# Optimization experiments

Hardware: AMD Instinct MI355X
Metric: run time of the kernel (lower is better)

Reference implementation:

```python
import jax, jax.numpy as jnp
import numpy as np

N_NODES = 50000
N_EDGES = 800000
IN_FEATS = 128
OUT_FEATS = 128
FREQ_DIM = OUT_FEATS // 2 + 1
BN_EPS = 1e-5


def setup_inputs() -> dict:
    key = jax.random.key(0)
    ks = jax.random.split(key, 8)
    x = jax.random.normal(ks[0], (N_NODES, IN_FEATS), dtype=jnp.float32)
    edge_index = jax.random.randint(ks[1], (2, N_EDGES), 0, N_NODES, dtype=jnp.int64)
    # lin_fusion: Linear(2*in_feats, out_feats)
    W_fuse = jax.random.normal(ks[2], (OUT_FEATS, 2 * IN_FEATS), dtype=jnp.float32) * (1.0 / np.sqrt(2 * IN_FEATS))
    b_fuse = jnp.zeros((OUT_FEATS,), dtype=jnp.float32)
    # lin_in: Linear(in_feats, out_feats)
    W_in = jax.random.normal(ks[3], (OUT_FEATS, IN_FEATS), dtype=jnp.float32) * (1.0 / np.sqrt(IN_FEATS))
    b_in = jnp.zeros((OUT_FEATS,), dtype=jnp.float32)
    complex_weight = jax.random.normal(ks[4], (FREQ_DIM, 2), dtype=jnp.float32) * 0.02
    alpha = jnp.float32(0.5)
    gamma = jnp.ones((OUT_FEATS,), dtype=jnp.float32)
    beta = jnp.zeros((OUT_FEATS,), dtype=jnp.float32)
    return {"x": x, "edge_index": edge_index, "W_fuse": W_fuse, "b_fuse": b_fuse,
            "W_in": W_in, "b_in": b_in, "complex_weight": complex_weight,
            "alpha": alpha, "gamma": gamma, "beta": beta}


def reference(x, edge_index, W_fuse, b_fuse, W_in, b_in, complex_weight, alpha, gamma, beta):
    N = x.shape[0]
    src, dst = edge_index[0], edge_index[1]
    # --- spatial branch: scatter-mean aggregation of neighbor features ---
    msgs = x[src]  # [E, in] gather
    agg_sum = jax.ops.segment_sum(msgs, dst, num_segments=N)  # [N, in]
    cnt = jax.ops.segment_sum(jnp.ones((src.shape[0],), dtype=x.dtype), dst, num_segments=N)
    aggs = agg_sum / jnp.maximum(cnt, 1.0)[:, None]
    combined = jnp.concatenate([x, aggs], axis=1)  # [N, 2*in]
    x_spatial = combined @ W_fuse.T + b_fuse  # [N, out]
    # --- spectral branch: linear -> rfft * complex weight -> irfft ---
    h = x @ W_in.T + b_in  # [N, out]
    hf = jnp.fft.rfft(h, axis=-1)  # [N, out//2+1]
    w = complex_weight[:, 0] + 1j * complex_weight[:, 1]
    x_spectral = jnp.fft.irfft(hf * w, n=h.shape[-1], axis=-1).astype(x.dtype)
    # --- fuse + BatchNorm1d (training stats, biased var) + exact GELU ---
    out = x_spatial + alpha * x_spectral
    mean = jnp.mean(out, axis=0)
    var = jnp.mean(jnp.square(out - mean), axis=0)
    out = (out - mean) / jnp.sqrt(var + BN_EPS) * gamma + beta
    return jax.nn.gelu(out, approximate=False)
```

## Files before the change

### kernel.cpp

```cpp
#include <hip/hip_runtime.h>
#include <hip/hip_bf16.h>

#define NN 50000
#define NE 800000
#define FD 128
#define FREQ 65
#define CAP 64
#define BN_EPS 1e-5f

#define NB_PACK 3125
#define NB_CVT  6250
#define NB_WCB  128
#define NGRP 8
#define GRPN 6250
#define NCHUNK 256
#define CHUNKE 3125

typedef unsigned int u32;
typedef unsigned short u16;
typedef __attribute__((ext_vector_type(8))) short short8;
typedef __attribute__((ext_vector_type(4))) float float4v;
typedef __attribute__((ext_vector_type(2))) float floatx2;

__device__ __forceinline__ float bf2f(u16 v) {
    return __uint_as_float(((u32)v) << 16);
}
__device__ __forceinline__ u16 f2bf(float f) {
    u32 u = __float_as_uint(f);
    u32 lsb = (u >> 16) & 1u;
    return (u16)((u + 0x7fffu + lsb) >> 16);
}
__device__ __forceinline__ float ldf(const void* p, int i, int f32) {
    return f32 ? ((const float*)p)[i] : bf2f(((const u16*)p)[i]);
}
__device__ __forceinline__ int detect_f32(const void* gamma) {
    return ((const u32*)gamma)[0] == 0x3F800000u;
}
__device__ __forceinline__ int detect_idx64(const int* idx) {
    return (idx[1] | idx[3] | idx[5] | idx[7] |
            idx[9] | idx[11] | idx[13] | idx[15]) == 0;
}

__device__ __forceinline__ u32 pk4_e4m3(float a, float b, float c, float d) {
#if __has_builtin(__builtin_amdgcn_cvt_pk_fp8_f32)
    int r = __builtin_amdgcn_cvt_pk_fp8_f32(a, b, 0, false);
    r = __builtin_amdgcn_cvt_pk_fp8_f32(c, d, r, true);
    return (u32)r;
#else
    auto one = [](float f) -> u32 {
        u32 u = __float_as_uint(f);
        u32 s = (u >> 24) & 0x80u;
        float af = fabsf(f);
        if (af > 448.f) return s | 0x7Eu;
        if (af < 7.8125e-3f) return s;
        int e = (int)((u >> 23) & 255) - 127;
        u32 m = (u >> 20) & 7u;
        u32 rnd = (u >> 19) & 1u;
        u32 sticky = (u & 0x7FFFFu) ? 1u : 0u;
        m += (rnd & (sticky | (m & 1u)));
        u32 ee = (u32)(e + 7);
        if (m > 7u) { m = 0u; ee += 1u; }
        if (ee > 15u) return s | 0x7Eu;
        return s | (ee << 3) | m;
    };
    return one(a) | (one(b) << 8) | (one(c) << 16) | (one(d) << 24);
#endif
}
__device__ __forceinline__ void deq4_e4m3(u32 p, float& a, float& b, float& c, float& d) {
#if __has_builtin(__builtin_amdgcn_cvt_pk_f32_fp8)
    floatx2 lo = __builtin_amdgcn_cvt_pk_f32_fp8((int)p, false);
    floatx2 hi = __builtin_amdgcn_cvt_pk_f32_fp8((int)p, true);
    a = lo.x; b = lo.y; c = hi.x; d = hi.y;
#else
    auto one = [](u32 v) -> float {
        u32 s = (v & 0x80u) << 24;
        u32 e = (v >> 3) & 15u;
        u32 m = v & 7u;
        if (e == 0) {
            float f = (float)m * 0.001953125f;
            return s ? -f : f;
        }
        return __uint_as_float(s | ((e + 120u) << 23) | (m << 20));
    };
    a = one(p & 255u); b = one((p >> 8) & 255u);
    c = one((p >> 16) & 255u); d = one(p >> 24);
#endif
}

#define WS_WCB       0
#define WS_BIAS      65536
#define WS_ZSTART    66048
#define WS_BNSUM     66048
#define WS_BNSQ      66560
#define WS_DEG       67072
#define WS_ZEND      267072
#define WS_CSR16     267136
#define WS_AGG16     6667136
#define WS_EPACK     6667136
#define WS_OUT16     19467136
#define WS_X8        19467136

__global__ __launch_bounds__(256) void prep_kernel(const void* __restrict__ x,
                                                   const int* __restrict__ idx,
                                                   const void* __restrict__ Wf,
                                                   const void* __restrict__ bfu,
                                                   const void* __restrict__ Wi,
                                                   const void* __restrict__ bi,
                                                   const void* __restrict__ cw,
                                                   const void* __restrict__ alpha_p,
                                                   const void* __restrict__ gamma,
                                                   u32* __restrict__ epack,
                                                   u32* __restrict__ x8,
                                                   u16* __restrict__ WcB,
                                                   float* __restrict__ bias) {
    int b = blockIdx.x;
    int t = threadIdx.x;
    if (b < NB_PACK) {
        int e = b * 256 + t;
        int src, dst;
        if (detect_idx64(idx)) { src = idx[2 * e]; dst = idx[2 * NE + 2 * e]; }
        else                   { src = idx[e];     dst = idx[NE + e]; }
        epack[e] = ((u32)dst << 16) | (u32)src;
        return;
    }
    b -= NB_PACK;
    if (b < NB_CVT) {
        int gid = b * 256 + t;
        float a, bb, c, d;
        if (detect_f32(gamma)) {
            float4 v = ((const float4*)x)[gid];
            a = v.x; bb = v.y; c = v.z; d = v.w;
        } else {
            uint2 v = ((const uint2*)x)[gid];
            a = bf2f((u16)(v.x & 0xffffu)); bb = bf2f((u16)(v.x >> 16));
            c = bf2f((u16)(v.y & 0xffffu)); d = bf2f((u16)(v.y >> 16));
        }
        x8[gid] = pk4_e4m3(a, bb, c, d);
        return;
    }
    b -= NB_CVT;
    int f32 = detect_f32(gamma);
    int j = b;
    __shared__ float wr[FREQ], wi[FREQ];
    __shared__ float cl[128];
    __shared__ float part[256];
    if (t < FREQ) { wr[t] = ldf(cw, 2 * t, f32); wi[t] = ldf(cw, 2 * t + 1, f32); }
    __syncthreads();
    if (t < 128) {
        float s = wr[0] + ((t & 1) ? -wr[64] : wr[64]);
        for (int f = 1; f < 64; ++f) {
            int ph = (f * t) & 127;
            float th = (float)ph * (6.283185307179586f / 128.f);
            float sn, cs;
            sincosf(th, &sn, &cs);
            s += 2.f * (wr[f] * cs - wi[f] * sn);
        }
        cl[t] = s * (1.f / 128.f);
    }
    __syncthreads();
    int k = t & 127, mh = t >> 7;
    float acc = 0.f;
    int m0 = mh * 64;
#pragma unroll 8
    for (int mm = 0; mm < 64; ++mm) {
        int m = m0 + mm;
        acc = fmaf(ldf(Wi, m * 128 + k, f32), cl[(j - m) & 127], acc);
    }
    part[t] = acc;
    __syncthreads();
    if (t < 128) {
        float al = ldf(alpha_p, 0, f32);
        int ct = j >> 4;
        float v = ldf(Wf, j * 256 + k, f32) + al * (part[k] + part[k + 128]);
        int off = (((ct * 8 + (k >> 5)) * 64) + ((k >> 3) & 3) * 16 + (j & 15)) * 8 + (k & 7);
        WcB[off] = f2bf(v);
        int k2 = k + 128;
        float v2 = ldf(Wf, j * 256 + k2, f32);
        int off2 = (((ct * 8 + (k2 >> 5)) * 64) + ((k2 >> 3) & 3) * 16 + (j & 15)) * 8 + (k2 & 7);
        WcB[off2] = f2bf(v2);
        if (j == 0) {
            float bacc = 0.f;
            for (int m = 0; m < 128; ++m)
                bacc = fmaf(ldf(bi, m, f32), cl[(t - m) & 127], bacc);
            bias[t] = ldf(bfu, t, f32) + al * bacc;
        }
    }
}

__global__ __launch_bounds__(256) void bucket8_kernel(const u32* __restrict__ epack,
                                                      int* __restrict__ deg,
                                                      u16* __restrict__ csr) {
    int g = blockIdx.x & (NGRP - 1);
    int chunk = blockIdx.x >> 3;
    u32 lo = (u32)(g * GRPN) << 16;
    u32 hi = (u32)((g + 1) * GRPN) << 16;
    int base = chunk * CHUNKE;
    for (int i = threadIdx.x; i < CHUNKE; i += 256) {
        u32 p = epack[base + i];
        if (p >= lo && p < hi) {
            int dst = (int)(p >> 16);
            int pos = atomicAdd(deg + dst, 1);
            if (pos < CAP) csr[dst * CAP + pos] = (u16)(p & 0xffffu);
        }
    }
}

__global__ __launch_bounds__(256) void aggregate_kernel(const u32* __restrict__ x8,
                                                        const u16* __restrict__ csr,
                                                        const int* __restrict__ deg,
                                                        u32* __restrict__ agg16) {
    int gid = blockIdx.x * 256 + threadIdx.x;
    int n = gid >> 6;
    int lane = gid & 63;
    if (n >= NN) return;
    int q = lane & 31;
    int half = lane >> 5;
    int s = n * CAP;
    int dcount = deg[n];
    int e = s + min(dcount, CAP);
    float a0 = 0.f, a1 = 0.f, a2 = 0.f, a3 = 0.f;
    int i = s + half;
    for (; i + 2 < e; i += 4) {
        int s0 = csr[i], s1 = csr[i + 2];
        u32 p0 = x8[(size_t)s0 * 32 + q];
        u32 p1 = x8[(size_t)s1 * 32 + q];
        float b0, b1, b2, b3, c0, c1, c2, c3;
        deq4_e4m3(p0, b0, b1, b2, b3);
        deq4_e4m3(p1, c0, c1, c2, c3);
        a0 += b0 + c0; a1 += b1 + c1; a2 += b2 + c2; a3 += b3 + c3;
    }
    if (i < e) {
        u32 p = x8[(size_t)csr[i] * 32 + q];
        float b0, b1, b2, b3;
        deq4_e4m3(p, b0, b1, b2, b3);
        a0 += b0; a1 += b1; a2 += b2; a3 += b3;
    }
    a0 += __shfl_xor(a0, 32); a1 += __shfl_xor(a1, 32);
    a2 += __shfl_xor(a2, 32); a3 += __shfl_xor(a3, 32);
    if (half == 0) {
        float rinv = 1.f / fmaxf((float)dcount, 1.f);
        uint2 w;
        w.x = (u32)f2bf(a0 * rinv) | ((u32)f2bf(a1 * rinv) << 16);
        w.y = (u32)f2bf(a2 * rinv) | ((u32)f2bf(a3 * rinv) << 16);
        ((uint2*)agg16)[(size_t)n * 32 + q] = w;
    }
}

__global__ __launch_bounds__(256) void gemm_kernel(const void* __restrict__ x,
                                                   const u16* __restrict__ agg16,
                                                   const void* __restrict__ gamma,
                                                   const u16* __restrict__ WcB,
                                                   const float* __restrict__ bias,
                                                   u16* __restrict__ outp16,
                                                   float* __restrict__ bnsum,
                                                   float* __restrict__ bnsq) {
    __shared__ float lsum[FD], lsq[FD];
    int t = threadIdx.x;
    if (t < FD) { lsum[t] = 0.f; lsq[t] = 0.f; }
    __syncthreads();
    int f32 = detect_f32(gamma);
    int wave = t >> 6;
    int lane = t & 63;
    int quad = lane >> 4;
    int lm = lane & 15;
    int n0 = blockIdx.x * 64;
    int nrow = n0 + wave * 16 + lm;
    bool avalid = (nrow < NN);

    float4v acc[8];
#pragma unroll
    for (int ct = 0; ct < 8; ++ct) acc[ct] = (float4v){0.f, 0.f, 0.f, 0.f};

    const short8* bp = (const short8*)WcB;
#pragma unroll
    for (int ks = 0; ks < 8; ++ks) {
        short8 a = (short8)0;
        if (avalid) {
            if (ks < 4) {
                int k = ks * 32 + quad * 8;
                if (f32) {
                    const float4* p = (const float4*)x + (size_t)nrow * 32 + (k >> 2);
                    float4 v0 = p[0], v1 = p[1];
                    a[0] = (short)f2bf(v0.x); a[1] = (short)f2bf(v0.y);
                    a[2] = (short)f2bf(v0.z); a[3] = (short)f2bf(v0.w);
                    a[4] = (short)f2bf(v1.x); a[5] = (short)f2bf(v1.y);
                    a[6] = (short)f2bf(v1.z); a[7] = (short)f2bf(v1.w);
                } else {
                    a = ((const short8*)x)[(size_t)nrow * 16 + (k >> 3)];
                }
            } else {
                int k = (ks - 4) * 32 + quad * 8;
                a = ((const short8*)agg16)[(size_t)nrow * 16 + (k >> 3)];
            }
        }
#pragma unroll
        for (int ct = 0; ct < 8; ++ct) {
            short8 b = bp[(ct * 8 + ks) * 64 + lane];
            acc[ct] = __builtin_amdgcn_mfma_f32_16x16x32_bf16(a, b, acc[ct], 0, 0, 0);
        }
    }

    int rbase = n0 + wave * 16 + quad * 4;
#pragma unroll
    for (int ct = 0; ct < 8; ++ct) {
        int col = ct * 16 + lm;
        float bj = bias[col];
        float s = 0.f, q = 0.f;
#pragma unroll
        for (int r = 0; r < 4; ++r) {
            int n = rbase + r;
            if (n < NN) {
                float v = acc[ct][r] + bj;
                outp16[(size_t)n * FD + col] = f2bf(v);
                s += v;
                q = fmaf(v, v, q);
            }
        }
        s += __shfl_xor(s, 16); s += __shfl_xor(s, 32);
        q += __shfl_xor(q, 16); q += __shfl_xor(q, 32);
        if (lane < 16) {
            atomicAdd(&lsum[col], s);
            atomicAdd(&lsq[col], q);
        }
    }
    __syncthreads();
    if (t < FD) {
        atomicAdd(bnsum + t, lsum[t]);
        atomicAdd(bnsq + t, lsq[t]);
    }
}

__global__ __launch_bounds__(256) void apply_kernel(const u32* __restrict__ outp16,
                                                    const float* __restrict__ bnsum,
                                                    const float* __restrict__ bnsq,
                                                    const void* __restrict__ gamma,
                                                    const void* __restrict__ beta,
                                                    void* __restrict__ out) {
    __shared__ float sc[FD], sh[FD];
    int t = threadIdx.x;
    int f32 = detect_f32(gamma);
    if (t < FD) {
        float mean = bnsum[t] * (1.f / NN);
        float var = bnsq[t] * (1.f / NN) - mean * mean;
        float s = ldf(gamma, t, f32) / sqrtf(var + BN_EPS);
        sc[t] = s;
        sh[t] = ldf(beta, t, f32) - mean * s;
    }
    __syncthreads();
    int gid = blockIdx.x * 256 + t;
    if (gid >= NN * (FD / 8)) return;
    uint4 pk = ((const uint4*)outp16)[gid];
    int f0 = (gid * 8) & 127;
    u32 w[4] = {pk.x, pk.y, pk.z, pk.w};
    float g[8];
#pragma unroll
    for (int q = 0; q < 4; ++q) {
        float v0 = bf2f((u16)(w[q] & 0xffffu));
        float v1 = bf2f((u16)(w[q] >> 16));
        float z0 = fmaf(v0, sc[f0 + 2 * q], sh[f0 + 2 * q]);
        float z1 = fmaf(v1, sc[f0 + 2 * q + 1], sh[f0 + 2 * q + 1]);
        g[2 * q]     = 0.5f * z0 * (1.f + erff(z0 * 0.70710678118654752f));
        g[2 * q + 1] = 0.5f * z1 * (1.f + erff(z1 * 0.70710678118654752f));
    }
    if (f32) {
        float4* o = (float4*)out + (size_t)gid * 2;
        o[0] = make_float4(g[0], g[1], g[2], g[3]);
        o[1] = make_float4(g[4], g[5], g[6], g[7]);
    } else {
        uint4 o;
        o.x = (u32)f2bf(g[0]) | ((u32)f2bf(g[1]) << 16);
        o.y = (u32)f2bf(g[2]) | ((u32)f2bf(g[3]) << 16);
        o.z = (u32)f2bf(g[4]) | ((u32)f2bf(g[5]) << 16);
        o.w = (u32)f2bf(g[6]) | ((u32)f2bf(g[7]) << 16);
        ((uint4*)out)[gid] = o;
    }
}

extern "C" void kernel_launch(void* const* d_in, const int* in_sizes, int n_in,
                              void* d_out, int out_size, void* d_ws, size_t ws_size,
                              hipStream_t stream) {
    const void* x     = d_in[0];
    const int* eidx   = (const int*)d_in[1];
    const void* Wf    = d_in[2];
    const void* bfu   = d_in[3];
    const void* Wi    = d_in[4];
    const void* bi    = d_in[5];
    const void* cw    = d_in[6];
    const void* alpha = d_in[7];
    const void* gamma = d_in[8];
    const void* beta  = d_in[9];

    char* ws = (char*)d_ws;
    u16*   WcB    = (u16*)(ws + WS_WCB);
    float* bias   = (float*)(ws + WS_BIAS);
    float* bnsum  = (float*)(ws + WS_BNSUM);
    float* bnsq   = (float*)(ws + WS_BNSQ);
    int*   deg    = (int*)(ws + WS_DEG);
    u16*   csr    = (u16*)(ws + WS_CSR16);
    u32*   epack  = (u32*)(ws + WS_EPACK);
    u32*   agg16  = (u32*)(ws + WS_AGG16);
    u16*   outp16 = (u16*)(ws + WS_OUT16);
    u32*   x8     = (u32*)(ws + WS_X8);

    hipMemsetAsync(ws + WS_ZSTART, 0, (size_t)WS_ZEND - WS_ZSTART, stream);

    prep_kernel<<<NB_PACK + NB_CVT + NB_WCB, 256, 0, stream>>>(
        x, eidx, Wf, bfu, Wi, bi, cw, alpha, gamma, epack, x8, WcB, bias);
    bucket8_kernel<<<NGRP * NCHUNK, 256, 0, stream>>>(epack, deg, csr);
    aggregate_kernel<<<(NN * 64 + 255) / 256, 256, 0, stream>>>(x8, csr, deg, agg16);
    gemm_kernel<<<(NN + 63) / 64, 256, 0, stream>>>(x, (const u16*)agg16, gamma, WcB,
                                                    bias, outp16, bnsum, bnsq);
    apply_kernel<<<(NN * (FD / 8) + 255) / 256, 256, 0, stream>>>((const u32*)outp16,
                                                                  bnsum, bnsq, gamma,
                                                                  beta, d_out);
}
```

Measured before the change: 236.3 us.

## Fuse neighbor aggregation into GEMM kernel via shared-memory staging

Removes the separate aggregate kernel and computes the mean-aggregated neighbor features inside the GEMM block, staging the bf16 results in LDS instead of writing and re-reading them from global memory. CSR indices are loaded once per wave row and broadcast with shuffles, and eight gathers are issued before any dequantization to raise memory-level parallelism. This saves one launch and the agg16 round trip. The cost is lower parallelism for the gather phase (782 blocks, each wave handling 8 nodes serially per half) plus 16KB of LDS per block, which may reduce occupancy.

```diff
diff --git a/kernel.cpp b/kernel.cpp
--- a/kernel.cpp
+++ b/kernel.cpp
@@ -95,10 +95,9 @@
 #define WS_DEG       67072
 #define WS_ZEND      267072
 #define WS_CSR16     267136
-#define WS_AGG16     6667136
 #define WS_EPACK     6667136
-#define WS_OUT16     19467136
-#define WS_X8        19467136
+#define WS_X8        9867136
+#define WS_OUT16     16267136
 
 __global__ __launch_bounds__(256) void prep_kernel(const void* __restrict__ x,
                                                    const int* __restrict__ idx,
@@ -205,49 +204,10 @@
     }
 }
 
-__global__ __launch_bounds__(256) void aggregate_kernel(const u32* __restrict__ x8,
-                                                        const u16* __restrict__ csr,
-                                                        const int* __restrict__ deg,
-                                                        u32* __restrict__ agg16) {
-    int gid = blockIdx.x * 256 + threadIdx.x;
-    int n = gid >> 6;
-    int lane = gid & 63;
-    if (n >= NN) return;
-    int q = lane & 31;
-    int half = lane >> 5;
-    int s = n * CAP;
-    int dcount = deg[n];
-    int e = s + min(dcount, CAP);
-    float a0 = 0.f, a1 = 0.f, a2 = 0.f, a3 = 0.f;
-    int i = s + half;
-    for (; i + 2 < e; i += 4) {
-        int s0 = csr[i], s1 = csr[i + 2];
-        u32 p0 = x8[(size_t)s0 * 32 + q];
-        u32 p1 = x8[(size_t)s1 * 32 + q];
-        float b0, b1, b2, b3, c0, c1, c2, c3;
-        deq4_e4m3(p0, b0, b1, b2, b3);
-        deq4_e4m3(p1, c0, c1, c2, c3);
-        a0 += b0 + c0; a1 += b1 + c1; a2 += b2 + c2; a3 += b3 + c3;
-    }
-    if (i < e) {
-        u32 p = x8[(size_t)csr[i] * 32 + q];
-        float b0, b1, b2, b3;
-        deq4_e4m3(p, b0, b1, b2, b3);
-        a0 += b0; a1 += b1; a2 += b2; a3 += b3;
-    }
-    a0 += __shfl_xor(a0, 32); a1 += __shfl_xor(a1, 32);
-    a2 += __shfl_xor(a2, 32); a3 += __shfl_xor(a3, 32);
-    if (half == 0) {
-        float rinv = 1.f / fmaxf((float)dcount, 1.f);
-        uint2 w;
-        w.x = (u32)f2bf(a0 * rinv) | ((u32)f2bf(a1 * rinv) << 16);
-        w.y = (u32)f2bf(a2 * rinv) | ((u32)f2bf(a3 * rinv) << 16);
-        ((uint2*)agg16)[(size_t)n * 32 + q] = w;
-    }
-}
-
 __global__ __launch_bounds__(256) void gemm_kernel(const void* __restrict__ x,
-                                                   const u16* __restrict__ agg16,
+                                                   const u32* __restrict__ x8,
+                                                   const u16* __restrict__ csr,
+                                                   const int* __restrict__ deg,
                                                    const void* __restrict__ gamma,
                                                    const u16* __restrict__ WcB,
                                                    const float* __restrict__ bias,
@@ -255,15 +215,61 @@
                                                    float* __restrict__ bnsum,
                                                    float* __restrict__ bnsq) {
     __shared__ float lsum[FD], lsq[FD];
+    __shared__ __align__(16) u16 lag[64 * FD];
     int t = threadIdx.x;
     if (t < FD) { lsum[t] = 0.f; lsq[t] = 0.f; }
-    __syncthreads();
     int f32 = detect_f32(gamma);
     int wave = t >> 6;
     int lane = t & 63;
+    int n0 = blockIdx.x * 64;
+
+    {
+        int half = lane >> 5;
+        int q = lane & 31;
+        for (int nn = 0; nn < 8; ++nn) {
+            int lrow = wave * 16 + half * 8 + nn;
+            int node = n0 + lrow;
+            int dcount = 0;
+            u32 cv = 0;
+            if (node < NN) {
+                dcount = deg[node];
+                cv = ((const u32*)csr)[(size_t)node * (CAP / 2) + q];
+            }
+            int cnt = min(dcount, CAP);
+            float a0 = 0.f, a1 = 0.f, a2 = 0.f, a3 = 0.f;
+            int jj = 0;
+            while (jj < cnt) {
+                int nb = cnt - jj;
+                u32 p[8];
+#pragma unroll
+                for (int r = 0; r < 8; ++r) {
+                    if (r < nb) {
+                        u32 w = __shfl(cv, half * 32 + ((jj + r) >> 1));
+                        u16 srcn = (u16)(w >> (((jj + r) & 1) * 16));
+                        p[r] = x8[(size_t)srcn * 32 + q];
+                    }
+                }
+#pragma unroll
+                for (int r = 0; r < 8; ++r) {
+                    if (r < nb) {
+                        float b0, b1, b2, b3;
+                        deq4_e4m3(p[r], b0, b1, b2, b3);
+                        a0 += b0; a1 += b1; a2 += b2; a3 += b3;
+                    }
+                }
+                jj += 8;
+            }
+            float rinv = 1.f / fmaxf((float)dcount, 1.f);
+            uint2 w;
+            w.x = (u32)f2bf(a0 * rinv) | ((u32)f2bf(a1 * rinv) << 16);
+            w.y = (u32)f2bf(a2 * rinv) | ((u32)f2bf(a3 * rinv) << 16);
+            ((uint2*)lag)[lrow * 32 + q] = w;
+        }
+    }
+    __syncthreads();
+
     int quad = lane >> 4;
     int lm = lane & 15;
-    int n0 = blockIdx.x * 64;
     int nrow = n0 + wave * 16 + lm;
     bool avalid = (nrow < NN);
 
@@ -275,8 +281,8 @@
 #pragma unroll
     for (int ks = 0; ks < 8; ++ks) {
         short8 a = (short8)0;
-        if (avalid) {
-            if (ks < 4) {
+        if (ks < 4) {
+            if (avalid) {
                 int k = ks * 32 + quad * 8;
                 if (f32) {
                     const float4* p = (const float4*)x + (size_t)nrow * 32 + (k >> 2);
@@ -288,10 +294,10 @@
                 } else {
                     a = ((const short8*)x)[(size_t)nrow * 16 + (k >> 3)];
                 }
-            } else {
-                int k = (ks - 4) * 32 + quad * 8;
-                a = ((const short8*)agg16)[(size_t)nrow * 16 + (k >> 3)];
             }
+        } else {
+            int k = (ks - 4) * 32 + quad * 8;
+            a = *(const short8*)&lag[(wave * 16 + lm) * FD + k];
         }
 #pragma unroll
         for (int ct = 0; ct < 8; ++ct) {
@@ -398,17 +404,15 @@
     int*   deg    = (int*)(ws + WS_DEG);
     u16*   csr    = (u16*)(ws + WS_CSR16);
     u32*   epack  = (u32*)(ws + WS_EPACK);
-    u32*   agg16  = (u32*)(ws + WS_AGG16);
+    u32*   x8     = (u32*)(ws + WS_X8);
     u16*   outp16 = (u16*)(ws + WS_OUT16);
-    u32*   x8     = (u32*)(ws + WS_X8);
 
     hipMemsetAsync(ws + WS_ZSTART, 0, (size_t)WS_ZEND - WS_ZSTART, stream);
 
     prep_kernel<<<NB_PACK + NB_CVT + NB_WCB, 256, 0, stream>>>(
         x, eidx, Wf, bfu, Wi, bi, cw, alpha, gamma, epack, x8, WcB, bias);
     bucket8_kernel<<<NGRP * NCHUNK, 256, 0, stream>>>(epack, deg, csr);
-    aggregate_kernel<<<(NN * 64 + 255) / 256, 256, 0, stream>>>(x8, csr, deg, agg16);
-    gemm_kernel<<<(NN + 63) / 64, 256, 0, stream>>>(x, (const u16*)agg16, gamma, WcB,
+    gemm_kernel<<<(NN + 63) / 64, 256, 0, stream>>>(x, x8, csr, deg, gamma, WcB,
                                                     bias, outp16, bnsum, bnsq);
     apply_kernel<<<(NN * (FD / 8) + 255) / 256, 256, 0, stream>>>((const u32*)outp16,
                                                                   bnsum, bnsq, gamma,
```

New measurement: 251.8 us. 6.6% more time.

## Preload CSR row via wave shuffle and batch 8 gathers with zero sentinel row

Applied to the files above, without the earlier changes.

The aggregate kernel now loads each node's whole 64-entry CSR row with one coalesced 32-bit load per lane and hands neighbor indices out with shuffles. Eight x8 gathers are issued before any dequantization, and padding slots point at an all-zero sentinel row that an extra memset clears, so the loop needs no tail handling. The workspace is rearranged so x8, agg16 and outp16 no longer alias, which the sentinel row requires. The aim is more memory-level parallelism in the gather. In exchange, nodes whose degree is not a multiple of 16 fetch extra sentinel rows.

```diff
diff --git a/kernel.cpp b/kernel.cpp
--- a/kernel.cpp
+++ b/kernel.cpp
@@ -15,6 +15,7 @@
 #define GRPN 6250
 #define NCHUNK 256
 #define CHUNKE 3125
+#define SENT NN
 
 typedef unsigned int u32;
 typedef unsigned short u16;
@@ -95,10 +96,10 @@
 #define WS_DEG       67072
 #define WS_ZEND      267072
 #define WS_CSR16     267136
-#define WS_AGG16     6667136
 #define WS_EPACK     6667136
-#define WS_OUT16     19467136
-#define WS_X8        19467136
+#define WS_X8        9867136
+#define WS_AGG16     16267264
+#define WS_OUT16     29067264
 
 __global__ __launch_bounds__(256) void prep_kernel(const void* __restrict__ x,
                                                    const int* __restrict__ idx,
@@ -211,34 +212,39 @@
                                                         u32* __restrict__ agg16) {
     int gid = blockIdx.x * 256 + threadIdx.x;
     int n = gid >> 6;
-    int lane = gid & 63;
+    int lane = threadIdx.x & 63;
     if (n >= NN) return;
     int q = lane & 31;
-    int half = lane >> 5;
-    int s = n * CAP;
-    int dcount = deg[n];
-    int e = s + min(dcount, CAP);
+    int h = lane >> 5;
+    const u32* csrw = (const u32*)csr;
+    int dc = deg[n];
+    int cnt = min(dc, CAP);
+    u32 cv = csrw[(size_t)n * (CAP / 2) + q];
+    u32 e0 = (2 * q     < cnt) ? (cv & 0xffffu) : (u32)SENT;
+    u32 e1 = (2 * q + 1 < cnt) ? (cv >> 16)     : (u32)SENT;
+    cv = e0 | (e1 << 16);
+
     float a0 = 0.f, a1 = 0.f, a2 = 0.f, a3 = 0.f;
-    int i = s + half;
-    for (; i + 2 < e; i += 4) {
-        int s0 = csr[i], s1 = csr[i + 2];
-        u32 p0 = x8[(size_t)s0 * 32 + q];
-        u32 p1 = x8[(size_t)s1 * 32 + q];
-        float b0, b1, b2, b3, c0, c1, c2, c3;
-        deq4_e4m3(p0, b0, b1, b2, b3);
-        deq4_e4m3(p1, c0, c1, c2, c3);
-        a0 += b0 + c0; a1 += b1 + c1; a2 += b2 + c2; a3 += b3 + c3;
-    }
-    if (i < e) {
-        u32 p = x8[(size_t)csr[i] * 32 + q];
-        float b0, b1, b2, b3;
-        deq4_e4m3(p, b0, b1, b2, b3);
-        a0 += b0; a1 += b1; a2 += b2; a3 += b3;
+    for (int jj = 0; jj < cnt; jj += 16) {
+        u32 p[8];
+#pragma unroll
+        for (int r = 0; r < 8; ++r) {
+            int i = jj + 2 * r + h;
+            u32 w = __shfl(cv, i >> 1);
+            u32 s = (i & 1) ? (w >> 16) : (w & 0xffffu);
+            p[r] = x8[(size_t)s * 32 + q];
+        }
+#pragma unroll
+        for (int r = 0; r < 8; ++r) {
+            float b0, b1, b2, b3;
+            deq4_e4m3(p[r], b0, b1, b2, b3);
+            a0 += b0; a1 += b1; a2 += b2; a3 += b3;
+        }
     }
     a0 += __shfl_xor(a0, 32); a1 += __shfl_xor(a1, 32);
     a2 += __shfl_xor(a2, 32); a3 += __shfl_xor(a3, 32);
-    if (half == 0) {
-        float rinv = 1.f / fmaxf((float)dcount, 1.f);
+    if (h == 0) {
+        float rinv = 1.f / fmaxf((float)dc, 1.f);
         uint2 w;
         w.x = (u32)f2bf(a0 * rinv) | ((u32)f2bf(a1 * rinv) << 16);
         w.y = (u32)f2bf(a2 * rinv) | ((u32)f2bf(a3 * rinv) << 16);
@@ -398,11 +404,12 @@
     int*   deg    = (int*)(ws + WS_DEG);
     u16*   csr    = (u16*)(ws + WS_CSR16);
     u32*   epack  = (u32*)(ws + WS_EPACK);
+    u32*   x8     = (u32*)(ws + WS_X8);
     u32*   agg16  = (u32*)(ws + WS_AGG16);
     u16*   outp16 = (u16*)(ws + WS_OUT16);
-    u32*   x8     = (u32*)(ws + WS_X8);
 
     hipMemsetAsync(ws + WS_ZSTART, 0, (size_t)WS_ZEND - WS_ZSTART, stream);
+    hipMemsetAsync(ws + WS_X8 + (size_t)NN * FD, 0, FD, stream);
 
     prep_kernel<<<NB_PACK + NB_CVT + NB_WCB, 256, 0, stream>>>(
         x, eidx, Wf, bfu, Wi, bi, cw, alpha, gamma, epack, x8, WcB, bias);
```

Result: faster. 228.7 us (-3.2%).
